# Kernel tuning notes

Hardware: AMD Instinct MI355X
Metric: run time of the kernel (lower is better)

The kernel has to match this reference:

```python
import jax, jax.numpy as jnp
import numpy as np

SCALING = 32.0 / 16.0  # lora_alpha / r

def setup_inputs() -> dict:
    key = jax.random.key(0)
    ks = jax.random.split(key, 7)
    B, T, D, O, R, E = 4, 2048, 4096, 4096, 16, 8
    x = jax.random.normal(ks[0], (B, T, D), dtype=jnp.float32)
    base_W = jax.random.normal(ks[1], (O, D), dtype=jnp.float32) * (D ** -0.5)
    base_b = jax.random.normal(ks[2], (O,), dtype=jnp.float32) * 0.01
    router_W = jax.random.normal(ks[3], (2 * E - 1, D), dtype=jnp.float32) * (D ** -0.5)
    router_b = jax.random.normal(ks[4], (2 * E - 1,), dtype=jnp.float32) * 0.01
    A = jax.random.normal(ks[5], (E, R, D), dtype=jnp.float32) * (D ** -0.5)
    Bm = jax.random.normal(ks[6], (E, O, R), dtype=jnp.float32) * (R ** -0.5)
    assigned_idx = 0
    others = [i for i in range(E) if i != assigned_idx]
    expert_map = jnp.array([assigned_idx] * E + others, dtype=jnp.int32)
    return {"x": x, "base_W": base_W, "base_b": base_b,
            "router_W": router_W, "router_b": router_b,
            "A": A, "B": Bm, "expert_map": expert_map}

def reference(x, base_W, base_b, router_W, router_b, A, B, expert_map):
    E = A.shape[0]
    # base linear
    base_out = jnp.einsum('btd,od->bto', x, base_W) + base_b
    # router of the assigned expert (2E-1 logits), softmax, top-k with k=E
    logits = jnp.einsum('btd,nd->btn', x, router_W) + router_b
    probs = jax.nn.softmax(logits, axis=-1)
    topk_p, topk_i = jax.lax.top_k(probs, E)           # [B,T,E]
    mapped = expert_map[topk_i]                        # [B,T,E] expert ids
    # per-expert combine weight: sum of top-k probs routed to expert e
    onehot = (mapped[..., None] == jnp.arange(E)).astype(x.dtype)  # [B,T,K,E]
    w = jnp.einsum('btk,btke->bte', topk_p, onehot)    # [B,T,E]
    # LoRA experts: weight * B(A(x)); scale low-rank h by w (linearity)
    h = jnp.einsum('btd,erd->bter', x, A)              # [B,T,E,r]
    lora = jnp.einsum('bter,eor->bto', h * w[..., None], B) * SCALING
    return base_out + lora
```

## Files before the change

### kernel.cpp

```cpp
#include <hip/hip_runtime.h>
#include <cstdint>

typedef unsigned short u16;
typedef short s16x8 __attribute__((ext_vector_type(8)));
typedef float f32x4 __attribute__((ext_vector_type(4)));
typedef unsigned short u16x4 __attribute__((ext_vector_type(4)));

#define KX    4096
#define BT    8192
#define OUT_D 4096
#define NW    4224

__device__ __forceinline__ u16 bf16_rne(float v) {
  unsigned u = __float_as_uint(v);
  return (u16)((u + 0x7FFFu + ((u >> 16) & 1u)) >> 16);
}
__device__ __forceinline__ float bf16_f(u16 h) { return __uint_as_float(((unsigned)h) << 16); }

__device__ __forceinline__ void gl16(const void* g, void* l) {
  auto gp = reinterpret_cast<const __attribute__((address_space(1))) unsigned int*>(
      reinterpret_cast<uintptr_t>(g));
  auto lp = reinterpret_cast<__attribute__((address_space(3))) unsigned int*>(
      reinterpret_cast<uintptr_t>(l));
  __builtin_amdgcn_global_load_lds(gp, lp, 16, 0, 0);
}

__device__ __forceinline__ void route_w(const float* s, const float* rb,
                                        const int* emap, float* wsc, int t) {
  float p[15]; float mx = -1e30f;
#pragma unroll
  for (int i = 0; i < 15; ++i) { p[i] = s[i] + rb[i]; mx = fmaxf(mx, p[i]); }
  float sum = 0.f;
#pragma unroll
  for (int i = 0; i < 15; ++i) { p[i] = __expf(p[i] - mx); sum += p[i]; }
  const float inv = 1.f / sum;
  float w[8] = {0, 0, 0, 0, 0, 0, 0, 0};
  unsigned sel = 0;
  for (int j = 0; j < 8; ++j) {
    int bi = -1; float bv = -1.f;
    for (int i = 0; i < 15; ++i)
      if (!((sel >> i) & 1u) && p[i] > bv) { bv = p[i]; bi = i; }
    sel |= 1u << bi;
    w[emap[bi]] += p[bi] * inv;
  }
#pragma unroll
  for (int e = 0; e < 8; ++e) wsc[t * 8 + e] = w[e] * 2.0f;
}

__global__ __launch_bounds__(256) void k_split_x(
    const float* __restrict__ x, const float* __restrict__ rW, const float* __restrict__ rb,
    const int* __restrict__ emap,
    u16* __restrict__ Xh, u16* __restrict__ Xl, float* __restrict__ wsc)
{
  const int tid = threadIdx.x;
  const int blk = blockIdx.x;

  const float4* xs = (const float4*)x + (size_t)blk * 8192;
#pragma unroll 4
  for (int j = 0; j < 32; ++j) {
    const int i = j * 256 + tid;
    float4 v = xs[i];
    float vv[4] = {v.x, v.y, v.z, v.w};
    u16x4 hv, lv;
#pragma unroll
    for (int q = 0; q < 4; ++q) {
      u16 h = bf16_rne(vv[q]);
      hv[q] = h; lv[q] = bf16_rne(vv[q] - bf16_f(h));
    }
    const size_t e0 = ((size_t)blk * 8192 + i) * 4;
    *(u16x4*)&Xh[e0] = hv;
    *(u16x4*)&Xl[e0] = lv;
  }

  const int lane = tid & 63, wid = tid >> 6;
  const int t0 = blk * 8 + wid * 2;
  const float4* xr0 = (const float4*)x + (size_t)t0 * 1024;
  const float4* xr1 = xr0 + 1024;
  const float4* w4 = (const float4*)rW;
  float s0[15], s1[15];
#pragma unroll
  for (int o = 0; o < 15; ++o) { s0[o] = 0.f; s1[o] = 0.f; }
  for (int it = 0; it < 16; ++it) {
    const int off = it * 64 + lane;
    float4 xa = xr0[off];
    float4 xb = xr1[off];
#pragma unroll
    for (int o = 0; o < 15; ++o) {
      float4 w = w4[o * 1024 + off];
      s0[o] = fmaf(xa.x, w.x, fmaf(xa.y, w.y, fmaf(xa.z, w.z, fmaf(xa.w, w.w, s0[o]))));
      s1[o] = fmaf(xb.x, w.x, fmaf(xb.y, w.y, fmaf(xb.z, w.z, fmaf(xb.w, w.w, s1[o]))));
    }
  }
#pragma unroll
  for (int o = 0; o < 15; ++o) {
#pragma unroll
    for (int d = 32; d; d >>= 1) {
      s0[o] += __shfl_down(s0[o], d, 64);
      s1[o] += __shfl_down(s1[o], d, 64);
    }
  }
  if (lane == 0) {
    route_w(s0, rb, emap, wsc, t0);
    route_w(s1, rb, emap, wsc, t0 + 1);
  }
}

__global__ __launch_bounds__(256) void k_split_w(
    const float* __restrict__ bW, const float* __restrict__ A,
    u16* __restrict__ dh, u16* __restrict__ dl)
{
  const long n4 = (long)NW * KX / 4;
  for (long i = (long)blockIdx.x * 256 + threadIdx.x; i < n4; i += (long)gridDim.x * 256) {
    float4 v = (i < 4194304) ? ((const float4*)bW)[i] : ((const float4*)A)[i - 4194304];
    float vv[4] = {v.x, v.y, v.z, v.w};
    u16x4 hv, lv;
#pragma unroll
    for (int j = 0; j < 4; ++j) {
      u16 h = bf16_rne(vv[j]);
      hv[j] = h; lv[j] = bf16_rne(vv[j] - bf16_f(h));
    }
    *(u16x4*)&dh[i * 4] = hv;
    *(u16x4*)&dl[i * 4] = lv;
  }
}

__global__ __launch_bounds__(256) void k_bt(
    const float* __restrict__ B, u16* __restrict__ dh, u16* __restrict__ dl,
    float* __restrict__ btf, int fast)
{
  const int idx = blockIdx.x * 256 + threadIdx.x;
  if (idx >= 8 * 4096 * 16) return;
  const int e = idx >> 16;
  const int o = (idx >> 4) & 4095;
  const int r = idx & 15;
  const float v = B[idx];
  const int off = o * 128 + e * 16 + r;
  if (fast) {
    u16 h = bf16_rne(v);
    dh[off] = h; dl[off] = bf16_rne(v - bf16_f(h));
  } else {
    btf[off] = v;
  }
}

__global__ __launch_bounds__(256) void k_gemm1(
    const u16* __restrict__ Xh, const u16* __restrict__ Xl,
    const u16* __restrict__ Wh, const u16* __restrict__ Wl,
    const float* __restrict__ bias, const float* __restrict__ wsc,
    float* __restrict__ out, u16* __restrict__ XLh, u16* __restrict__ XLl)
{
  __shared__ __align__(16) u16 lAh[4096], lAl[4096], lBh[4096], lBl[4096];
  const int tid = threadIdx.x;
  const int lane = tid & 63;
  const int wid = tid >> 6;

  const int bI = blockIdx.x;
  const int cpx = gridDim.x >> 3;
  const int wg = (bI & 7) * cpx + (bI >> 3);
  const int bm = wg / 33;
  const int bn = wg % 33;
  const int wr = wid >> 1, wc = wid & 1;

  const int srow = tid >> 2;
  const int skc = (tid & 3) << 3;
  const size_t a0 = (size_t)(bm * 128 + srow) * KX + skc;
  const size_t a1 = a0 + (size_t)64 * KX;
  const size_t b0 = (size_t)(bn * 128 + srow) * KX + skc;
  const size_t b1 = b0 + (size_t)64 * KX;
  const int d0 = wid * 512;
  const int d1 = 2048 + wid * 512;

  const int ra = (wr * 64 + (lane & 15)) * 32 + ((lane >> 4) << 3);
  const int rb = (wc * 64 + (lane & 15)) * 32 + ((lane >> 4) << 3);

  f32x4 acc[4][4] = {};

  for (int kt = 0; kt < 128; ++kt) {
    const int ko = kt * 32;
    gl16(Xh + a0 + ko, lAh + d0);
    gl16(Xh + a1 + ko, lAh + d1);
    gl16(Xl + a0 + ko, lAl + d0);
    gl16(Xl + a1 + ko, lAl + d1);
    gl16(Wh + b0 + ko, lBh + d0);
    gl16(Wh + b1 + ko, lBh + d1);
    gl16(Wl + b0 + ko, lBl + d0);
    gl16(Wl + b1 + ko, lBl + d1);
    asm volatile("s_waitcnt vmcnt(0)" ::: "memory");
    __syncthreads();

    s16x8 ah[4], al[4], bh[4], bl[4];
#pragma unroll
    for (int m = 0; m < 4; ++m) {
      ah[m] = *(const s16x8*)&lAh[ra + m * 512];
      al[m] = *(const s16x8*)&lAl[ra + m * 512];
    }
#pragma unroll
    for (int n = 0; n < 4; ++n) {
      bh[n] = *(const s16x8*)&lBh[rb + n * 512];
      bl[n] = *(const s16x8*)&lBl[rb + n * 512];
    }
#pragma unroll
    for (int m = 0; m < 4; ++m)
#pragma unroll
      for (int n = 0; n < 4; ++n) {
        acc[m][n] = __builtin_amdgcn_mfma_f32_16x16x32_bf16(ah[m], bh[n], acc[m][n], 0, 0, 0);
        acc[m][n] = __builtin_amdgcn_mfma_f32_16x16x32_bf16(ah[m], bl[n], acc[m][n], 0, 0, 0);
        acc[m][n] = __builtin_amdgcn_mfma_f32_16x16x32_bf16(al[m], bh[n], acc[m][n], 0, 0, 0);
      }
    __syncthreads();
  }

  const int orow = bm * 128 + wr * 64 + ((lane >> 4) << 2);
  const int ocol = bn * 128 + wc * 64 + (lane & 15);
  if (bn < 32) {
#pragma unroll
    for (int n = 0; n < 4; ++n) {
      const float bv = bias[ocol + n * 16];
#pragma unroll
      for (int m = 0; m < 4; ++m)
#pragma unroll
        for (int r = 0; r < 4; ++r)
          out[(size_t)(orow + m * 16 + r) * OUT_D + ocol + n * 16] = acc[m][n][r] + bv;
    }
  } else {
#pragma unroll
    for (int n = 0; n < 4; ++n) {
      const int j = ocol + n * 16 - KX;
      const int e = j >> 4;
#pragma unroll
      for (int m = 0; m < 4; ++m)
#pragma unroll
        for (int r = 0; r < 4; ++r) {
          const int t = orow + m * 16 + r;
          const float v = acc[m][n][r] * wsc[t * 8 + e];
          u16 h = bf16_rne(v);
          XLh[t * 128 + j] = h;
          XLl[t * 128 + j] = bf16_rne(v - bf16_f(h));
        }
    }
  }
}

__global__ __launch_bounds__(256) void k_gemm2(
    const u16* __restrict__ XLh, const u16* __restrict__ XLl,
    const u16* __restrict__ Bth, const u16* __restrict__ Btl,
    float* __restrict__ out)
{
  __shared__ __align__(16) u16 lAh[4096], lAl[4096], lBh[4096], lBl[4096];
  const int tid = threadIdx.x;
  const int lane = tid & 63;
  const int wid = tid >> 6;

  const int bI = blockIdx.x;
  const int cpx = gridDim.x >> 3;
  const int wg = (bI & 7) * cpx + (bI >> 3);
  const int bm = wg >> 5;
  const int bn = wg & 31;
  const int wr = wid >> 1, wc = wid & 1;

  const int srow = tid >> 2;
  const int skc = (tid & 3) << 3;
  const size_t a0 = (size_t)(bm * 128 + srow) * 128 + skc;
  const size_t a1 = a0 + (size_t)64 * 128;
  const size_t b0 = (size_t)(bn * 128 + srow) * 128 + skc;
  const size_t b1 = b0 + (size_t)64 * 128;
  const int d0 = wid * 512;
  const int d1 = 2048 + wid * 512;

  const int ra = (wr * 64 + (lane & 15)) * 32 + ((lane >> 4) << 3);
  const int rb = (wc * 64 + (lane & 15)) * 32 + ((lane >> 4) << 3);

  f32x4 acc[4][4] = {};

  for (int kt = 0; kt < 4; ++kt) {
    const int ko = kt * 32;
    gl16(XLh + a0 + ko, lAh + d0);
    gl16(XLh + a1 + ko, lAh + d1);
    gl16(XLl + a0 + ko, lAl + d0);
    gl16(XLl + a1 + ko, lAl + d1);
    gl16(Bth + b0 + ko, lBh + d0);
    gl16(Bth + b1 + ko, lBh + d1);
    gl16(Btl + b0 + ko, lBl + d0);
    gl16(Btl + b1 + ko, lBl + d1);
    asm volatile("s_waitcnt vmcnt(0)" ::: "memory");
    __syncthreads();

    s16x8 ah[4], al[4], bh[4], bl[4];
#pragma unroll
    for (int m = 0; m < 4; ++m) {
      ah[m] = *(const s16x8*)&lAh[ra + m * 512];
      al[m] = *(const s16x8*)&lAl[ra + m * 512];
    }
#pragma unroll
    for (int n = 0; n < 4; ++n) {
      bh[n] = *(const s16x8*)&lBh[rb + n * 512];
      bl[n] = *(const s16x8*)&lBl[rb + n * 512];
    }
#pragma unroll
    for (int m = 0; m < 4; ++m)
#pragma unroll
      for (int n = 0; n < 4; ++n) {
        acc[m][n] = __builtin_amdgcn_mfma_f32_16x16x32_bf16(ah[m], bh[n], acc[m][n], 0, 0, 0);
        acc[m][n] = __builtin_amdgcn_mfma_f32_16x16x32_bf16(ah[m], bl[n], acc[m][n], 0, 0, 0);
        acc[m][n] = __builtin_amdgcn_mfma_f32_16x16x32_bf16(al[m], bh[n], acc[m][n], 0, 0, 0);
      }
    __syncthreads();
  }

  const int orow = bm * 128 + wr * 64 + ((lane >> 4) << 2);
  const int ocol = bn * 128 + wc * 64 + (lane & 15);
#pragma unroll
  for (int n = 0; n < 4; ++n)
#pragma unroll
    for (int m = 0; m < 4; ++m)
#pragma unroll
      for (int r = 0; r < 4; ++r) {
        const size_t o = (size_t)(orow + m * 16 + r) * OUT_D + ocol + n * 16;
        out[o] += acc[m][n][r];
      }
}

__global__ __launch_bounds__(256) void k_router_fb(
    const float* __restrict__ x, const float* __restrict__ rW, const float* __restrict__ rb,
    const float* __restrict__ A, const int* __restrict__ emap, float* __restrict__ hwf)
{
  __shared__ float4 xs4[1024];
  __shared__ float outs[144];
  __shared__ float wsc[8];
  const int t = blockIdx.x;
  const int tid = threadIdx.x;
  const float4* xr = (const float4*)(x + (size_t)t * 4096);
#pragma unroll
  for (int i = 0; i < 4; ++i) xs4[tid + i * 256] = xr[tid + i * 256];
  __syncthreads();

  const int lane = tid & 63, wid = tid >> 6;
  for (int o = wid; o < 143; o += 4) {
    const float4* wrow = (const float4*)((o < 15) ? (rW + (size_t)o * 4096)
                                                  : (A + (size_t)(o - 15) * 4096));
    float s = 0.f;
    for (int i = lane; i < 1024; i += 64) {
      float4 a = xs4[i];
      float4 w = wrow[i];
      s = fmaf(a.x, w.x, fmaf(a.y, w.y, fmaf(a.z, w.z, fmaf(a.w, w.w, s))));
    }
#pragma unroll
    for (int off = 32; off; off >>= 1) s += __shfl_down(s, off, 64);
    if (lane == 0) outs[o] = s + ((o < 15) ? rb[o] : 0.f);
  }
  __syncthreads();
  if (tid == 0) {
    float p[15];
    float mx = outs[0];
#pragma unroll
    for (int i = 1; i < 15; ++i) mx = fmaxf(mx, outs[i]);
    float sum = 0.f;
#pragma unroll
    for (int i = 0; i < 15; ++i) { p[i] = __expf(outs[i] - mx); sum += p[i]; }
    const float inv = 1.f / sum;
    float w[8] = {0, 0, 0, 0, 0, 0, 0, 0};
    unsigned sel = 0;
    for (int j = 0; j < 8; ++j) {
      int bi = -1; float bv = -1.f;
      for (int i = 0; i < 15; ++i)
        if (!((sel >> i) & 1u) && p[i] > bv) { bv = p[i]; bi = i; }
      sel |= 1u << bi;
      w[emap[bi]] += p[bi] * inv;
    }
#pragma unroll
    for (int e = 0; e < 8; ++e) wsc[e] = w[e] * 2.0f;
  }
  __syncthreads();
  if (tid < 128) hwf[(size_t)t * 128 + tid] = outs[15 + tid] * wsc[tid >> 4];
}

__global__ __launch_bounds__(256) void k_gemm_fb(
    const float* __restrict__ X, const float* __restrict__ W, const float* __restrict__ bias,
    const float* __restrict__ hwf, const float* __restrict__ btf, float* __restrict__ out)
{
  __shared__ float sA[64][33], sB[64][33];
  const int bm = blockIdx.x >> 6;
  const int bn = blockIdx.x & 63;
  const int tid = threadIdx.x;
  const int tr = tid >> 4, tc = tid & 15;
  float acc[4][4] = {};

  const float* Aps[2] = {X, hwf};
  const float* Bps[2] = {W, btf};
  const int lds_[2] = {4096, 128};
  const int Ks[2] = {4096, 128};

  for (int ph = 0; ph < 2; ++ph) {
    const float* Ap = Aps[ph];
    const float* Bp = Bps[ph];
    const int ld = lds_[ph];
    for (int k0 = 0; k0 < Ks[ph]; k0 += 32) {
      __syncthreads();
      for (int i = tid; i < 512; i += 256) {
        const int r = i >> 3, c = (i & 7) << 2;
        float4 va = *(const float4*)&Ap[(size_t)(bm * 64 + r) * ld + k0 + c];
        sA[r][c] = va.x; sA[r][c + 1] = va.y; sA[r][c + 2] = va.z; sA[r][c + 3] = va.w;
        float4 vb = *(const float4*)&Bp[(size_t)(bn * 64 + r) * ld + k0 + c];
        sB[r][c] = vb.x; sB[r][c + 1] = vb.y; sB[r][c + 2] = vb.z; sB[r][c + 3] = vb.w;
      }
      __syncthreads();
      for (int k = 0; k < 32; ++k) {
        float a[4], bvv[4];
#pragma unroll
        for (int i = 0; i < 4; ++i) a[i] = sA[tr * 4 + i][k];
#pragma unroll
        for (int j = 0; j < 4; ++j) bvv[j] = sB[tc * 4 + j][k];
#pragma unroll
        for (int i = 0; i < 4; ++i)
#pragma unroll
          for (int j = 0; j < 4; ++j) acc[i][j] = fmaf(a[i], bvv[j], acc[i][j]);
      }
    }
  }
#pragma unroll
  for (int i = 0; i < 4; ++i)
#pragma unroll
    for (int j = 0; j < 4; ++j)
      out[(size_t)(bm * 64 + tr * 4 + i) * OUT_D + bn * 64 + tc * 4 + j] =
          acc[i][j] + bias[bn * 64 + tc * 4 + j];
}

extern "C" void kernel_launch(void* const* d_in, const int* in_sizes, int n_in,
                              void* d_out, int out_size, void* d_ws, size_t ws_size,
                              hipStream_t stream) {
  const float* x    = (const float*)d_in[0];
  const float* bW   = (const float*)d_in[1];
  const float* bb   = (const float*)d_in[2];
  const float* rW   = (const float*)d_in[3];
  const float* rb   = (const float*)d_in[4];
  const float* A    = (const float*)d_in[5];
  const float* Bm   = (const float*)d_in[6];
  const int*   emap = (const int*)d_in[7];
  float* out = (float*)d_out;

  const size_t SZ_XH  = (size_t)BT * KX * 2;
  const size_t SZ_WH  = (size_t)NW * KX * 2;
  const size_t SZ_XL  = (size_t)BT * 128 * 2;
  const size_t SZ_BT  = (size_t)OUT_D * 128 * 2;
  const size_t SZ_WSC = (size_t)BT * 8 * 4;
  const size_t need = 2 * SZ_XH + 2 * SZ_WH + 2 * SZ_XL + 2 * SZ_BT + SZ_WSC;
  char* ws = (char*)d_ws;

  if (ws_size >= need) {
    u16* Xh  = (u16*)ws;
    u16* Xl  = (u16*)(ws + SZ_XH);
    u16* Wh  = (u16*)(ws + 2 * SZ_XH);
    u16* Wl  = (u16*)(ws + 2 * SZ_XH + SZ_WH);
    u16* XLh = (u16*)(ws + 2 * SZ_XH + 2 * SZ_WH);
    u16* XLl = (u16*)(ws + 2 * SZ_XH + 2 * SZ_WH + SZ_XL);
    u16* Bth = (u16*)(ws + 2 * SZ_XH + 2 * SZ_WH + 2 * SZ_XL);
    u16* Btl = (u16*)(ws + 2 * SZ_XH + 2 * SZ_WH + 2 * SZ_XL + SZ_BT);
    float* wsc = (float*)(ws + 2 * SZ_XH + 2 * SZ_WH + 2 * SZ_XL + 2 * SZ_BT);

    k_split_w<<<dim3(4224), dim3(256), 0, stream>>>(bW, A, Wh, Wl);
    k_split_x<<<dim3(1024), dim3(256), 0, stream>>>(x, rW, rb, emap, Xh, Xl, wsc);
    k_bt<<<dim3(2048), dim3(256), 0, stream>>>(Bm, Bth, Btl, nullptr, 1);
    k_gemm1<<<dim3(2112), dim3(256), 0, stream>>>(Xh, Xl, Wh, Wl, bb, wsc, out, XLh, XLl);
    k_gemm2<<<dim3(2048), dim3(256), 0, stream>>>(XLh, XLl, Bth, Btl, out);
  } else {
    float* hwf = (float*)ws;
    float* btf = (float*)(ws + (size_t)BT * 128 * 4);
    k_router_fb<<<dim3(BT), dim3(256), 0, stream>>>(x, rW, rb, A, emap, hwf);
    k_bt<<<dim3(2048), dim3(256), 0, stream>>>(Bm, nullptr, nullptr, btf, 0);
    k_gemm_fb<<<dim3(8192), dim3(256), 0, stream>>>(x, bW, bb, hwf, btf, out);
  }
}
```

Baseline: 1.498 ms.

## Rewrite gemm1 with 256x256 tiles, double-buffered LDS pipeline and swizzle

The main split-bf16 GEMM now uses 512-thread blocks computing 256x256 tiles, with double-buffered LDS staging so loads for the next k-step are issued between MFMA groups. It adds an XOR swizzle on LDS columns and s_setprio around MFMA bursts. The goal is to raise arithmetic intensity, hide global-load latency and cut LDS bank conflicts. The trade-offs are more registers and LDS per block and a partly wasted final column tile, since only 128 of the 256 LoRA columns are used.

```diff
diff --git a/kernel.cpp b/kernel.cpp
--- a/kernel.cpp
+++ b/kernel.cpp
@@ -24,6 +24,8 @@
       reinterpret_cast<uintptr_t>(l));
   __builtin_amdgcn_global_load_lds(gp, lp, 16, 0, 0);
 }
+
+#define MFMA(a, b, c) __builtin_amdgcn_mfma_f32_16x16x32_bf16((a), (b), (c), 0, 0, 0)
 
 __device__ __forceinline__ void route_w(const float* s, const float* rb,
                                         const int* emap, float* wsc, int t) {
@@ -143,102 +145,207 @@
   }
 }
 
-__global__ __launch_bounds__(256) void k_gemm1(
+__global__ __launch_bounds__(512, 2) void k_gemm1(
     const u16* __restrict__ Xh, const u16* __restrict__ Xl,
     const u16* __restrict__ Wh, const u16* __restrict__ Wl,
     const float* __restrict__ bias, const float* __restrict__ wsc,
     float* __restrict__ out, u16* __restrict__ XLh, u16* __restrict__ XLl)
 {
-  __shared__ __align__(16) u16 lAh[4096], lAl[4096], lBh[4096], lBl[4096];
+  __shared__ __align__(16) u16 lds[2][4][8192];
   const int tid = threadIdx.x;
   const int lane = tid & 63;
   const int wid = tid >> 6;
+  const int l15 = lane & 15;
+  const int wr = wid >> 2;
+  const int wc = wid & 3;
 
   const int bI = blockIdx.x;
   const int cpx = gridDim.x >> 3;
   const int wg = (bI & 7) * cpx + (bI >> 3);
-  const int bm = wg / 33;
-  const int bn = wg % 33;
-  const int wr = wid >> 1, wc = wid & 1;
-
-  const int srow = tid >> 2;
-  const int skc = (tid & 3) << 3;
-  const size_t a0 = (size_t)(bm * 128 + srow) * KX + skc;
-  const size_t a1 = a0 + (size_t)64 * KX;
-  const size_t b0 = (size_t)(bn * 128 + srow) * KX + skc;
-  const size_t b1 = b0 + (size_t)64 * KX;
-  const int d0 = wid * 512;
-  const int d1 = 2048 + wid * 512;
-
-  const int ra = (wr * 64 + (lane & 15)) * 32 + ((lane >> 4) << 3);
-  const int rb = (wc * 64 + (lane & 15)) * 32 + ((lane >> 4) << 3);
-
-  f32x4 acc[4][4] = {};
-
-  for (int kt = 0; kt < 128; ++kt) {
-    const int ko = kt * 32;
-    gl16(Xh + a0 + ko, lAh + d0);
-    gl16(Xh + a1 + ko, lAh + d1);
-    gl16(Xl + a0 + ko, lAl + d0);
-    gl16(Xl + a1 + ko, lAl + d1);
-    gl16(Wh + b0 + ko, lBh + d0);
-    gl16(Wh + b1 + ko, lBh + d1);
-    gl16(Wl + b0 + ko, lBl + d0);
-    gl16(Wl + b1 + ko, lBl + d1);
+  const int bm = wg / 17;
+  const int bn = wg % 17;
+
+  const size_t kcs = (size_t)(((tid & 3) ^ ((tid >> 3) & 3)) << 3);
+  const size_t offA0 = (size_t)(bm * 256 + (tid >> 2)) * KX + kcs;
+  const size_t offA1 = offA0 + (size_t)128 * KX;
+  const size_t offB0 = (size_t)(bn * 256 + (tid >> 2)) * KX + kcs;
+  const size_t offB1 = offB0 + (size_t)128 * KX;
+  const int ldsw = wid * 512;
+
+#define STG(buf, p, P, o0, o1, kb)                       \
+  gl16(P + (o0) + (kb), &lds[buf][p][ldsw]);             \
+  gl16(P + (o1) + (kb), &lds[buf][p][4096 + ldsw]);
+
+  const int swk = ((lane >> 4) ^ ((l15 >> 1) & 3)) << 3;
+  const int aBase = (wr * 128 + l15) * 32 + swk;
+  const int bBase = (wc * 64 + l15) * 32 + swk;
+
+  f32x4 acc[8][4] = {};
+
+  STG(0, 0, Xh, offA0, offA1, 0);
+  STG(0, 1, Wh, offB0, offB1, 0);
+  STG(0, 3, Wl, offB0, offB1, 0);
+  STG(0, 2, Xl, offA0, offA1, 0);
+
+  int cur = 0;
+  for (int st = 0; st < 127; ++st) {
+    const int nxt = cur ^ 1;
+    const size_t kb = (size_t)(st + 1) * 32;
+    const u16* Ah_ = lds[cur][0];
+    const u16* Bh_ = lds[cur][1];
+    const u16* Al_ = lds[cur][2];
+    const u16* Bl_ = lds[cur][3];
+
+    asm volatile("s_waitcnt vmcnt(4)" ::: "memory");
+    asm volatile("s_barrier" ::: "memory");
+    STG(nxt, 0, Xh, offA0, offA1, kb);
+    s16x8 ah[8];
+#pragma unroll
+    for (int m = 0; m < 8; ++m) ah[m] = *(const s16x8*)&Ah_[aBase + m * 512];
+    s16x8 bh0 = *(const s16x8*)&Bh_[bBase];
+    s16x8 bh1 = *(const s16x8*)&Bh_[bBase + 512];
+    __builtin_amdgcn_s_setprio(1);
+#pragma unroll
+    for (int m = 0; m < 8; ++m) acc[m][0] = MFMA(ah[m], bh0, acc[m][0]);
+#pragma unroll
+    for (int m = 0; m < 8; ++m) acc[m][1] = MFMA(ah[m], bh1, acc[m][1]);
+    __builtin_amdgcn_s_setprio(0);
+
+    STG(nxt, 1, Wh, offB0, offB1, kb);
+    s16x8 bh2 = *(const s16x8*)&Bh_[bBase + 1024];
+    s16x8 bh3 = *(const s16x8*)&Bh_[bBase + 1536];
+    __builtin_amdgcn_s_setprio(1);
+#pragma unroll
+    for (int m = 0; m < 8; ++m) acc[m][2] = MFMA(ah[m], bh2, acc[m][2]);
+#pragma unroll
+    for (int m = 0; m < 8; ++m) acc[m][3] = MFMA(ah[m], bh3, acc[m][3]);
+    __builtin_amdgcn_s_setprio(0);
+
+    asm volatile("s_waitcnt vmcnt(4)" ::: "memory");
+    asm volatile("s_barrier" ::: "memory");
+    STG(nxt, 3, Wl, offB0, offB1, kb);
+    {
+      s16x8 bl0 = *(const s16x8*)&Bl_[bBase];
+      s16x8 bl1 = *(const s16x8*)&Bl_[bBase + 512];
+      __builtin_amdgcn_s_setprio(1);
+#pragma unroll
+      for (int m = 0; m < 8; ++m) acc[m][0] = MFMA(ah[m], bl0, acc[m][0]);
+#pragma unroll
+      for (int m = 0; m < 8; ++m) acc[m][1] = MFMA(ah[m], bl1, acc[m][1]);
+      __builtin_amdgcn_s_setprio(0);
+    }
+
+    STG(nxt, 2, Xl, offA0, offA1, kb);
+    {
+      s16x8 bl2 = *(const s16x8*)&Bl_[bBase + 1024];
+      s16x8 bl3 = *(const s16x8*)&Bl_[bBase + 1536];
+      __builtin_amdgcn_s_setprio(1);
+#pragma unroll
+      for (int m = 0; m < 8; ++m) acc[m][2] = MFMA(ah[m], bl2, acc[m][2]);
+#pragma unroll
+      for (int m = 0; m < 8; ++m) acc[m][3] = MFMA(ah[m], bl3, acc[m][3]);
+      __builtin_amdgcn_s_setprio(0);
+    }
+
+    {
+      s16x8 al[8];
+#pragma unroll
+      for (int m = 0; m < 8; ++m) al[m] = *(const s16x8*)&Al_[aBase + m * 512];
+      __builtin_amdgcn_s_setprio(1);
+#pragma unroll
+      for (int m = 0; m < 8; ++m) acc[m][0] = MFMA(al[m], bh0, acc[m][0]);
+#pragma unroll
+      for (int m = 0; m < 8; ++m) acc[m][1] = MFMA(al[m], bh1, acc[m][1]);
+#pragma unroll
+      for (int m = 0; m < 8; ++m) acc[m][2] = MFMA(al[m], bh2, acc[m][2]);
+#pragma unroll
+      for (int m = 0; m < 8; ++m) acc[m][3] = MFMA(al[m], bh3, acc[m][3]);
+      __builtin_amdgcn_s_setprio(0);
+    }
+    cur = nxt;
+  }
+
+  {
+    const u16* Ah_ = lds[cur][0];
+    const u16* Bh_ = lds[cur][1];
+    const u16* Al_ = lds[cur][2];
+    const u16* Bl_ = lds[cur][3];
+    asm volatile("s_waitcnt vmcnt(4)" ::: "memory");
+    asm volatile("s_barrier" ::: "memory");
+    s16x8 ah[8];
+#pragma unroll
+    for (int m = 0; m < 8; ++m) ah[m] = *(const s16x8*)&Ah_[aBase + m * 512];
+    s16x8 bh0 = *(const s16x8*)&Bh_[bBase];
+    s16x8 bh1 = *(const s16x8*)&Bh_[bBase + 512];
+    s16x8 bh2 = *(const s16x8*)&Bh_[bBase + 1024];
+    s16x8 bh3 = *(const s16x8*)&Bh_[bBase + 1536];
+#pragma unroll
+    for (int m = 0; m < 8; ++m) acc[m][0] = MFMA(ah[m], bh0, acc[m][0]);
+#pragma unroll
+    for (int m = 0; m < 8; ++m) acc[m][1] = MFMA(ah[m], bh1, acc[m][1]);
+#pragma unroll
+    for (int m = 0; m < 8; ++m) acc[m][2] = MFMA(ah[m], bh2, acc[m][2]);
+#pragma unroll
+    for (int m = 0; m < 8; ++m) acc[m][3] = MFMA(ah[m], bh3, acc[m][3]);
+    asm volatile("s_waitcnt vmcnt(2)" ::: "memory");
+    asm volatile("s_barrier" ::: "memory");
+#pragma unroll
+    for (int n = 0; n < 4; ++n) {
+      s16x8 bl = *(const s16x8*)&Bl_[bBase + n * 512];
+#pragma unroll
+      for (int m = 0; m < 8; ++m) acc[m][n] = MFMA(ah[m], bl, acc[m][n]);
+    }
     asm volatile("s_waitcnt vmcnt(0)" ::: "memory");
-    __syncthreads();
-
-    s16x8 ah[4], al[4], bh[4], bl[4];
-#pragma unroll
-    for (int m = 0; m < 4; ++m) {
-      ah[m] = *(const s16x8*)&lAh[ra + m * 512];
-      al[m] = *(const s16x8*)&lAl[ra + m * 512];
-    }
+    asm volatile("s_barrier" ::: "memory");
+    {
+      s16x8 al[8];
+#pragma unroll
+      for (int m = 0; m < 8; ++m) al[m] = *(const s16x8*)&Al_[aBase + m * 512];
+#pragma unroll
+      for (int m = 0; m < 8; ++m) acc[m][0] = MFMA(al[m], bh0, acc[m][0]);
+#pragma unroll
+      for (int m = 0; m < 8; ++m) acc[m][1] = MFMA(al[m], bh1, acc[m][1]);
+#pragma unroll
+      for (int m = 0; m < 8; ++m) acc[m][2] = MFMA(al[m], bh2, acc[m][2]);
+#pragma unroll
+      for (int m = 0; m < 8; ++m) acc[m][3] = MFMA(al[m], bh3, acc[m][3]);
+    }
+  }
+
+  const int orow0 = bm * 256 + wr * 128 + ((lane >> 4) << 2);
+  if (bn < 16) {
+    const int ocol0 = bn * 256 + wc * 64 + l15;
 #pragma unroll
     for (int n = 0; n < 4; ++n) {
-      bh[n] = *(const s16x8*)&lBh[rb + n * 512];
-      bl[n] = *(const s16x8*)&lBl[rb + n * 512];
-    }
-#pragma unroll
-    for (int m = 0; m < 4; ++m)
-#pragma unroll
-      for (int n = 0; n < 4; ++n) {
-        acc[m][n] = __builtin_amdgcn_mfma_f32_16x16x32_bf16(ah[m], bh[n], acc[m][n], 0, 0, 0);
-        acc[m][n] = __builtin_amdgcn_mfma_f32_16x16x32_bf16(ah[m], bl[n], acc[m][n], 0, 0, 0);
-        acc[m][n] = __builtin_amdgcn_mfma_f32_16x16x32_bf16(al[m], bh[n], acc[m][n], 0, 0, 0);
+      const int col = ocol0 + n * 16;
+      const float bv = bias[col];
+#pragma unroll
+      for (int m = 0; m < 8; ++m)
+#pragma unroll
+        for (int r = 0; r < 4; ++r)
+          out[(size_t)(orow0 + m * 16 + r) * OUT_D + col] = acc[m][n][r] + bv;
+    }
+  } else {
+    const int j0 = wc * 64 + l15;
+#pragma unroll
+    for (int n = 0; n < 4; ++n) {
+      const int j = j0 + n * 16;
+      if (j < 128) {
+        const int e = j >> 4;
+#pragma unroll
+        for (int m = 0; m < 8; ++m)
+#pragma unroll
+          for (int r = 0; r < 4; ++r) {
+            const int t = orow0 + m * 16 + r;
+            const float v = acc[m][n][r] * wsc[t * 8 + e];
+            u16 h = bf16_rne(v);
+            XLh[t * 128 + j] = h;
+            XLl[t * 128 + j] = bf16_rne(v - bf16_f(h));
+          }
       }
-    __syncthreads();
-  }
-
-  const int orow = bm * 128 + wr * 64 + ((lane >> 4) << 2);
-  const int ocol = bn * 128 + wc * 64 + (lane & 15);
-  if (bn < 32) {
-#pragma unroll
-    for (int n = 0; n < 4; ++n) {
-      const float bv = bias[ocol + n * 16];
-#pragma unroll
-      for (int m = 0; m < 4; ++m)
-#pragma unroll
-        for (int r = 0; r < 4; ++r)
-          out[(size_t)(orow + m * 16 + r) * OUT_D + ocol + n * 16] = acc[m][n][r] + bv;
-    }
-  } else {
-#pragma unroll
-    for (int n = 0; n < 4; ++n) {
-      const int j = ocol + n * 16 - KX;
-      const int e = j >> 4;
-#pragma unroll
-      for (int m = 0; m < 4; ++m)
-#pragma unroll
-        for (int r = 0; r < 4; ++r) {
-          const int t = orow + m * 16 + r;
-          const float v = acc[m][n][r] * wsc[t * 8 + e];
-          u16 h = bf16_rne(v);
-          XLh[t * 128 + j] = h;
-          XLl[t * 128 + j] = bf16_rne(v - bf16_f(h));
-        }
-    }
-  }
+    }
+  }
+#undef STG
 }
 
 __global__ __launch_bounds__(256) void k_gemm2(
@@ -300,9 +407,9 @@
     for (int m = 0; m < 4; ++m)
 #pragma unroll
       for (int n = 0; n < 4; ++n) {
-        acc[m][n] = __builtin_amdgcn_mfma_f32_16x16x32_bf16(ah[m], bh[n], acc[m][n], 0, 0, 0);
-        acc[m][n] = __builtin_amdgcn_mfma_f32_16x16x32_bf16(ah[m], bl[n], acc[m][n], 0, 0, 0);
-        acc[m][n] = __builtin_amdgcn_mfma_f32_16x16x32_bf16(al[m], bh[n], acc[m][n], 0, 0, 0);
+        acc[m][n] = MFMA(ah[m], bh[n], acc[m][n]);
+        acc[m][n] = MFMA(ah[m], bl[n], acc[m][n]);
+        acc[m][n] = MFMA(al[m], bh[n], acc[m][n]);
       }
     __syncthreads();
   }
@@ -460,7 +567,7 @@
     k_split_w<<<dim3(4224), dim3(256), 0, stream>>>(bW, A, Wh, Wl);
     k_split_x<<<dim3(1024), dim3(256), 0, stream>>>(x, rW, rb, emap, Xh, Xl, wsc);
     k_bt<<<dim3(2048), dim3(256), 0, stream>>>(Bm, Bth, Btl, nullptr, 1);
-    k_gemm1<<<dim3(2112), dim3(256), 0, stream>>>(Xh, Xl, Wh, Wl, bb, wsc, out, XLh, XLl);
+    k_gemm1<<<dim3(544), dim3(512), 0, stream>>>(Xh, Xl, Wh, Wl, bb, wsc, out, XLh, XLl);
     k_gemm2<<<dim3(2048), dim3(256), 0, stream>>>(XLh, XLl, Bth, Btl, out);
   } else {
     float* hwf = (float*)ws;
```

New measurement: 1.280 ms. -14.5%, faster.
